# Performance work log

Hardware: AMD Instinct MI355X
Metric: run time of the kernel (lower is better)

The kernel has to match this reference:

```python
import jax, jax.numpy as jnp
import numpy as np

H = 16          # nhead
EPS = 1e-5      # LayerNorm eps (torch default)


def _layernorm(x, g, b):
    mu = jnp.mean(x, axis=-1, keepdims=True)
    var = jnp.mean(jnp.square(x - mu), axis=-1, keepdims=True)
    return (x - mu) * jax.lax.rsqrt(var + EPS) * g + b


def setup_inputs() -> dict:
    key = jax.random.key(0)
    ks = jax.random.split(key, 8)
    B, L, D, F = 256, 64, 1024, 4096
    s = 0.02
    return {
        "src": jax.random.normal(ks[0], (B, L, D), jnp.float32),
        "Wq": jax.random.normal(ks[1], (D, D), jnp.float32) * s,
        "bq": jnp.zeros((D,), jnp.float32),
        "Wk": jax.random.normal(ks[2], (D, D), jnp.float32) * s,
        "bk": jnp.zeros((D,), jnp.float32),
        "Wv": jax.random.normal(ks[3], (D, D), jnp.float32) * s,
        "bv": jnp.zeros((D,), jnp.float32),
        "Wo": jax.random.normal(ks[4], (D, D), jnp.float32) * s,
        "bo": jnp.zeros((D,), jnp.float32),
        "rel_bias": jax.random.normal(ks[5], (H, 2 * L - 1), jnp.float32) * s,
        "W1": jax.random.normal(ks[6], (D, F), jnp.float32) * s,
        "b1": jnp.zeros((F,), jnp.float32),
        "W2": jax.random.normal(ks[7], (F, D), jnp.float32) * s,
        "b2": jnp.zeros((D,), jnp.float32),
        "g1": jnp.ones((D,), jnp.float32),
        "be1": jnp.zeros((D,), jnp.float32),
        "g2": jnp.ones((D,), jnp.float32),
        "be2": jnp.zeros((D,), jnp.float32),
    }


def reference(src, Wq, bq, Wk, bk, Wv, bv, Wo, bo, rel_bias,
              W1, b1, W2, b2, g1, be1, g2, be2):
    B, L, D = src.shape
    dh = D // H
    # --- relative multi-head attention ---
    q = (src @ Wq + bq).reshape(B, L, H, dh)
    k = (src @ Wk + bk).reshape(B, L, H, dh)
    v = (src @ Wv + bv).reshape(B, L, H, dh)
    scores = jnp.einsum('bqhd,bkhd->bhqk', q, k) / jnp.sqrt(jnp.float32(dh))
    # relative position bias lookup: index i - j + (L-1) into (H, 2L-1) table
    rel_idx = jnp.arange(L)[:, None] - jnp.arange(L)[None, :] + (L - 1)  # (L,L)
    scores = scores + rel_bias[:, rel_idx]  # broadcast (H,L,L) over batch
    attn = jax.nn.softmax(scores, axis=-1)
    ctx = jnp.einsum('bhqk,bkhd->bqhd', attn, v).reshape(B, L, D)
    attn_out = ctx @ Wo + bo
    # --- residual + LN + FFN + residual + LN (dropout = eval no-op) ---
    x = _layernorm(src + attn_out, g1, be1)
    ff = jax.nn.gelu(x @ W1 + b1) @ W2 + b2
    return _layernorm(x + ff, g2, be2)
```

## Files before the change

### kernel.cpp

```cpp
#include <hip/hip_runtime.h>

typedef __bf16 bf16;
typedef __attribute__((ext_vector_type(8))) __bf16 bf16x8;
typedef __attribute__((ext_vector_type(4))) __bf16 bf16x4;
typedef __attribute__((ext_vector_type(4))) float f32x4;

#define N_TOK 16384
#define DMODEL 1024
#define FDIM 4096
#define NHEAD 16

__device__ __forceinline__ void gload_lds16(const bf16* g, bf16* l) {
  __builtin_amdgcn_global_load_lds(
      (const __attribute__((address_space(1))) void*)g,
      (__attribute__((address_space(3))) void*)l,
      16, 0, 0);
}

__device__ __forceinline__ float gelu_tanh(float x) {
  return 0.5f * x * (1.0f + tanhf(0.7978845608028654f * (x + 0.044715f * x * x * x)));
}

__global__ __launch_bounds__(256) void cvt_copy(const float* __restrict__ x,
                                                bf16* __restrict__ y) {
  size_t i = ((size_t)blockIdx.x * 256 + threadIdx.x) * 8;
  float4 a = *(const float4*)(x + i);
  float4 b = *(const float4*)(x + i + 4);
  bf16x8 o;
  o[0] = (bf16)a.x; o[1] = (bf16)a.y; o[2] = (bf16)a.z; o[3] = (bf16)a.w;
  o[4] = (bf16)b.x; o[5] = (bf16)b.y; o[6] = (bf16)b.z; o[7] = (bf16)b.w;
  *(bf16x8*)(y + i) = o;
}

__global__ void convt(const float* __restrict__ src, bf16* __restrict__ dst,
                      int R, int C) {
  __shared__ float tile[32][33];
  int c0 = blockIdx.x * 32, r0 = blockIdx.y * 32;
  int tx = threadIdx.x, ty = threadIdx.y;
#pragma unroll
  for (int i = 0; i < 4; ++i)
    tile[ty * 4 + i][tx] = src[(size_t)(r0 + ty * 4 + i) * C + c0 + tx];
  __syncthreads();
#pragma unroll
  for (int i = 0; i < 4; ++i)
    dst[(size_t)(c0 + ty * 4 + i) * R + r0 + tx] = (bf16)tile[tx][ty * 4 + i];
}

template <int BM_, int RES, int GELU>
__global__ __launch_bounds__(512) void gemm_c(
    const bf16* __restrict__ A, const bf16* __restrict__ BT,
    const float* __restrict__ bias, const float* __restrict__ resf,
    const bf16* __restrict__ resb, bf16* __restrict__ C,
    int M, int N, int K) {
  constexpr int ALOADS = BM_ / 64;
  constexpr int MH = BM_ / 32;
  constexpr int MQ = MH / 2;
  __shared__ alignas(16) bf16 sA[2][BM_ * 64];
  __shared__ alignas(16) bf16 sB[2][256 * 64];

  const int tid = threadIdx.x;
  const int lane = tid & 63, wv = tid >> 6;
  const int wr = wv >> 2, wc = wv & 3;
  const int r16 = lane & 15, hk = lane >> 4;

  const int nbn = N >> 8;
  const int cpx = gridDim.x >> 3;
  const int swz = ((int)blockIdx.x & 7) * cpx + ((int)blockIdx.x >> 3);
  const int row0 = (swz / nbn) * BM_, col0 = (swz % nbn) << 8;

  const bf16* Ab = A + (size_t)row0 * K;
  const bf16* Bb = BT + (size_t)col0 * K;

  auto stageA = [&](int buf, int kt) {
#pragma unroll
    for (int l = 0; l < ALOADS; ++l) {
      int g = l * 512 + tid;
      int r = g >> 3, p = g & 7;
      gload_lds16(Ab + (size_t)r * K + ((size_t)kt << 6) + ((p ^ (r & 7)) << 3),
                  &sA[buf][g * 8]);
    }
  };
  auto stageB = [&](int buf, int kt) {
#pragma unroll
    for (int l = 0; l < 4; ++l) {
      int g = l * 512 + tid;
      int r = g >> 3, p = g & 7;
      gload_lds16(Bb + (size_t)r * K + ((size_t)kt << 6) + ((p ^ (r & 7)) << 3),
                  &sB[buf][g * 8]);
    }
  };
  auto frag = [&](const bf16* s, int row, int kc) -> bf16x8 {
    return *(const bf16x8*)(s + row * 64 + (kc ^ ((row & 7) * 8)));
  };

  f32x4 acc[MH][4] = {};
  bf16x8 aF[MQ][2], bF0[2][2], bF1[2][2];

  const int nt = K >> 6;
  stageA(0, 0); stageB(0, 0);
  stageA(1, 1); stageB(1, 1);
  if constexpr (BM_ == 256) asm volatile("s_waitcnt vmcnt(8)" ::: "memory");
  else                      asm volatile("s_waitcnt vmcnt(6)" ::: "memory");
  __builtin_amdgcn_s_barrier();

  for (int kt = 0; kt < nt; ++kt) {
    const int cb = kt & 1;
    const bf16* sa = &sA[cb][0];
    const bf16* sb = &sB[cb][0];
    const bool pf = (kt + 2 < nt);

#pragma unroll
    for (int m = 0; m < MQ; ++m)
#pragma unroll
      for (int ks = 0; ks < 2; ++ks)
        aF[m][ks] = frag(sa, wr * (BM_ / 2) + m * 16 + r16, ks * 32 + hk * 8);
#pragma unroll
    for (int n = 0; n < 2; ++n)
#pragma unroll
      for (int ks = 0; ks < 2; ++ks)
        bF0[n][ks] = frag(sb, wc * 64 + n * 16 + r16, ks * 32 + hk * 8);
    __builtin_amdgcn_s_barrier();
    __builtin_amdgcn_s_setprio(1);
#pragma unroll
    for (int m = 0; m < MQ; ++m)
#pragma unroll
      for (int n = 0; n < 2; ++n)
#pragma unroll
        for (int ks = 0; ks < 2; ++ks)
          acc[m][n] = __builtin_amdgcn_mfma_f32_16x16x32_bf16(bF0[n][ks], aF[m][ks], acc[m][n], 0, 0, 0);
    __builtin_amdgcn_s_setprio(0);
    __builtin_amdgcn_s_barrier();

#pragma unroll
    for (int n = 0; n < 2; ++n)
#pragma unroll
      for (int ks = 0; ks < 2; ++ks)
        bF1[n][ks] = frag(sb, wc * 64 + (2 + n) * 16 + r16, ks * 32 + hk * 8);
    __builtin_amdgcn_s_barrier();
    __builtin_amdgcn_s_setprio(1);
#pragma unroll
    for (int m = 0; m < MQ; ++m)
#pragma unroll
      for (int n = 0; n < 2; ++n)
#pragma unroll
        for (int ks = 0; ks < 2; ++ks)
          acc[m][2 + n] = __builtin_amdgcn_mfma_f32_16x16x32_bf16(bF1[n][ks], aF[m][ks], acc[m][2 + n], 0, 0, 0);
    __builtin_amdgcn_s_setprio(0);
    __builtin_amdgcn_s_barrier();

#pragma unroll
    for (int m = 0; m < MQ; ++m)
#pragma unroll
      for (int ks = 0; ks < 2; ++ks)
        aF[m][ks] = frag(sa, wr * (BM_ / 2) + (MQ + m) * 16 + r16, ks * 32 + hk * 8);
    if (pf) stageB(cb, kt + 2);
    __builtin_amdgcn_s_barrier();
    __builtin_amdgcn_s_setprio(1);
#pragma unroll
    for (int m = 0; m < MQ; ++m)
#pragma unroll
      for (int n = 0; n < 2; ++n)
#pragma unroll
        for (int ks = 0; ks < 2; ++ks)
          acc[MQ + m][2 + n] = __builtin_amdgcn_mfma_f32_16x16x32_bf16(bF1[n][ks], aF[m][ks], acc[MQ + m][2 + n], 0, 0, 0);
    __builtin_amdgcn_s_setprio(0);
    __builtin_amdgcn_s_barrier();

    if (pf) stageA(cb, kt + 2);
    __builtin_amdgcn_s_setprio(1);
#pragma unroll
    for (int m = 0; m < MQ; ++m)
#pragma unroll
      for (int n = 0; n < 2; ++n)
#pragma unroll
        for (int ks = 0; ks < 2; ++ks)
          acc[MQ + m][n] = __builtin_amdgcn_mfma_f32_16x16x32_bf16(bF0[n][ks], aF[m][ks], acc[MQ + m][n], 0, 0, 0);
    __builtin_amdgcn_s_setprio(0);
    if (pf) {
      if constexpr (BM_ == 256) asm volatile("s_waitcnt vmcnt(8)" ::: "memory");
      else                      asm volatile("s_waitcnt vmcnt(6)" ::: "memory");
    } else if (kt + 1 < nt) {
      asm volatile("s_waitcnt vmcnt(0)" ::: "memory");
    }
    __builtin_amdgcn_s_barrier();
  }

#pragma unroll
  for (int m = 0; m < MH; ++m) {
    int row = row0 + wr * (BM_ / 2) + m * 16 + r16;
#pragma unroll
    for (int n = 0; n < 4; ++n) {
      int col = col0 + wc * 64 + n * 16 + hk * 4;
      f32x4 b4 = *(const f32x4*)&bias[col];
      f32x4 v;
#pragma unroll
      for (int r = 0; r < 4; ++r) v[r] = acc[m][n][r] + b4[r];
      if (RES == 1) {
        f32x4 rr = *(const f32x4*)&resf[(size_t)row * N + col];
#pragma unroll
        for (int r = 0; r < 4; ++r) v[r] += rr[r];
      }
      if (RES == 2) {
        bf16x4 rb = *(const bf16x4*)&resb[(size_t)row * N + col];
#pragma unroll
        for (int r = 0; r < 4; ++r) v[r] += (float)rb[r];
      }
      bf16x4 o;
#pragma unroll
      for (int r = 0; r < 4; ++r) {
        float x = v[r];
        if (GELU) x = gelu_tanh(x);
        o[r] = (bf16)x;
      }
      *(bf16x4*)&C[(size_t)row * N + col] = o;
    }
  }
}

__global__ __launch_bounds__(256) void attn_k(
    const bf16* q, const bf16* __restrict__ k,
    const bf16* __restrict__ v, const float* __restrict__ rel,
    bf16* ctx) {
  __shared__ alignas(16) bf16 lQ[64 * 64];
  __shared__ alignas(16) bf16 lK[64 * 64];
  __shared__ alignas(16) bf16 lVt[64 * 64];
  __shared__ alignas(16) bf16 lP[4][16 * 64];
  __shared__ float lrel[128];

  const int bh = blockIdx.x;
  const int b = bh >> 4, h = bh & 15;
  const int tid = threadIdx.x;
  const size_t base = (size_t)(b * 64) * DMODEL + h * 64;

#pragma unroll
  for (int i = 0; i < 2; ++i) {
    int j = (tid >> 3) + i * 32;
    int d0 = (tid & 7) * 8;
    *(bf16x8*)&lQ[j * 64 + d0] = *(const bf16x8*)(q + base + (size_t)j * DMODEL + d0);
    *(bf16x8*)&lK[j * 64 + d0] = *(const bf16x8*)(k + base + (size_t)j * DMODEL + d0);
    bf16x8 vvv = *(const bf16x8*)(v + base + (size_t)j * DMODEL + d0);
#pragma unroll
    for (int u = 0; u < 8; ++u) lVt[(d0 + u) * 64 + j] = vvv[u];
  }
  if (tid < 127) lrel[tid] = rel[h * 127 + tid];
  __syncthreads();

  const int lane = tid & 63, w = tid >> 6;
  const int r16 = lane & 15, hk = lane >> 4;

  f32x4 s[4] = {};
#pragma unroll
  for (int dstep = 0; dstep < 2; ++dstep) {
    bf16x8 aq = *(const bf16x8*)&lQ[(w * 16 + r16) * 64 + dstep * 32 + hk * 8];
#pragma unroll
    for (int n = 0; n < 4; ++n) {
      bf16x8 bk_ = *(const bf16x8*)&lK[(n * 16 + r16) * 64 + dstep * 32 + hk * 8];
      s[n] = __builtin_amdgcn_mfma_f32_16x16x32_bf16(aq, bk_, s[n], 0, 0, 0);
    }
  }

  float p[16];
#pragma unroll
  for (int n = 0; n < 4; ++n)
#pragma unroll
    for (int r = 0; r < 4; ++r) {
      int i = w * 16 + hk * 4 + r;
      int j = n * 16 + r16;
      p[n * 4 + r] = s[n][r] * 0.125f + lrel[i - j + 63];
    }
#pragma unroll
  for (int r = 0; r < 4; ++r) {
    float m = fmaxf(fmaxf(p[r], p[4 + r]), fmaxf(p[8 + r], p[12 + r]));
#pragma unroll
    for (int off = 1; off < 16; off <<= 1) m = fmaxf(m, __shfl_xor(m, off));
    float sum = 0.f;
#pragma unroll
    for (int n = 0; n < 4; ++n) {
      p[n * 4 + r] = __expf(p[n * 4 + r] - m);
      sum += p[n * 4 + r];
    }
#pragma unroll
    for (int off = 1; off < 16; off <<= 1) sum += __shfl_xor(sum, off);
    float inv = 1.0f / sum;
#pragma unroll
    for (int n = 0; n < 4; ++n) p[n * 4 + r] *= inv;
  }
#pragma unroll
  for (int n = 0; n < 4; ++n)
#pragma unroll
    for (int r = 0; r < 4; ++r)
      lP[w][(hk * 4 + r) * 64 + n * 16 + r16] = (bf16)p[n * 4 + r];
  __syncthreads();

  f32x4 o[4] = {};
#pragma unroll
  for (int ks = 0; ks < 2; ++ks) {
    bf16x8 ap = *(const bf16x8*)&lP[w][r16 * 64 + ks * 32 + hk * 8];
#pragma unroll
    for (int n = 0; n < 4; ++n) {
      bf16x8 bv_ = *(const bf16x8*)&lVt[(n * 16 + r16) * 64 + ks * 32 + hk * 8];
      o[n] = __builtin_amdgcn_mfma_f32_16x16x32_bf16(ap, bv_, o[n], 0, 0, 0);
    }
  }
#pragma unroll
  for (int n = 0; n < 4; ++n)
#pragma unroll
    for (int r = 0; r < 4; ++r) {
      int trow = b * 64 + w * 16 + hk * 4 + r;
      ctx[(size_t)trow * DMODEL + h * 64 + n * 16 + r16] = (bf16)o[n][r];
    }
}

template <int F32OUT>
__global__ __launch_bounds__(256) void layernorm_k(
    const bf16* __restrict__ x, const float* __restrict__ g,
    const float* __restrict__ be, bf16* __restrict__ ob,
    float* __restrict__ of) {
  int row = blockIdx.x * 4 + (threadIdx.x >> 6);
  int lane = threadIdx.x & 63;
  const bf16* xr = x + (size_t)row * DMODEL + lane * 16;
  bf16x8 v0 = *(const bf16x8*)xr;
  bf16x8 v1 = *(const bf16x8*)(xr + 8);
  float f[16];
#pragma unroll
  for (int j = 0; j < 8; ++j) { f[j] = (float)v0[j]; f[8 + j] = (float)v1[j]; }
  float s = 0.f, sq = 0.f;
#pragma unroll
  for (int j = 0; j < 16; ++j) { s += f[j]; sq += f[j] * f[j]; }
#pragma unroll
  for (int off = 1; off < 64; off <<= 1) {
    s += __shfl_xor(s, off);
    sq += __shfl_xor(sq, off);
  }
  float mean = s * (1.0f / DMODEL);
  float var = sq * (1.0f / DMODEL) - mean * mean;
  float rstd = rsqrtf(var + 1e-5f);
  const float* gp = g + lane * 16;
  const float* bp = be + lane * 16;
  if (F32OUT) {
    float* op = of + (size_t)row * DMODEL + lane * 16;
#pragma unroll
    for (int j = 0; j < 16; ++j)
      op[j] = (f[j] - mean) * rstd * gp[j] + bp[j];
  } else {
    bf16x8 o0, o1;
#pragma unroll
    for (int j = 0; j < 8; ++j) {
      o0[j] = (bf16)((f[j] - mean) * rstd * gp[j] + bp[j]);
      o1[j] = (bf16)((f[8 + j] - mean) * rstd * gp[8 + j] + bp[8 + j]);
    }
    bf16* op = ob + (size_t)row * DMODEL + lane * 16;
    *(bf16x8*)op = o0;
    *(bf16x8*)(op + 8) = o1;
  }
}

extern "C" void kernel_launch(void* const* d_in, const int* in_sizes, int n_in,
                              void* d_out, int out_size, void* d_ws, size_t ws_size,
                              hipStream_t stream) {
  (void)in_sizes; (void)n_in; (void)out_size;
  const float* src = (const float*)d_in[0];
  const float* Wq  = (const float*)d_in[1];
  const float* bq  = (const float*)d_in[2];
  const float* Wk  = (const float*)d_in[3];
  const float* bk  = (const float*)d_in[4];
  const float* Wv  = (const float*)d_in[5];
  const float* bv  = (const float*)d_in[6];
  const float* Wo  = (const float*)d_in[7];
  const float* bo  = (const float*)d_in[8];
  const float* rel = (const float*)d_in[9];
  const float* W1  = (const float*)d_in[10];
  const float* b1  = (const float*)d_in[11];
  const float* W2  = (const float*)d_in[12];
  const float* b2  = (const float*)d_in[13];
  const float* g1  = (const float*)d_in[14];
  const float* be1 = (const float*)d_in[15];
  const float* g2  = (const float*)d_in[16];
  const float* be2 = (const float*)d_in[17];

  char* ws = (char*)d_ws;
  const size_t MiB = 1ull << 20;
  bf16* srcb = (bf16*)(ws + 0 * MiB);
  bf16* qb   = (bf16*)(ws + 32 * MiB);
  bf16* WqT  = (bf16*)(ws + 64 * MiB);
  bf16* WkT  = (bf16*)(ws + 66 * MiB);
  bf16* WvT  = (bf16*)(ws + 68 * MiB);
  bf16* WoT  = (bf16*)(ws + 70 * MiB);
  bf16* W1T  = (bf16*)(ws + 72 * MiB);
  bf16* W2T  = (bf16*)(ws + 80 * MiB);
  bf16* hbuf = (bf16*)(ws + 0 * MiB);
  float* lnout = (float*)(ws + 0 * MiB);
  bf16* kb = (bf16*)d_out;
  bf16* vb = (bf16*)((char*)d_out + 32 * MiB);
  bf16* y1 = kb;
  bf16* xb = vb;
  const bool bigws = (ws_size >= 121 * MiB);
  bf16* y2 = bigws ? (bf16*)(ws + 88 * MiB) : kb;

  cvt_copy<<<(N_TOK * DMODEL) / 2048, 256, 0, stream>>>(src, srcb);
  dim3 tb(32, 8);
  convt<<<dim3(32, 32), tb, 0, stream>>>(Wq, WqT, 1024, 1024);
  convt<<<dim3(32, 32), tb, 0, stream>>>(Wk, WkT, 1024, 1024);
  convt<<<dim3(32, 32), tb, 0, stream>>>(Wv, WvT, 1024, 1024);
  convt<<<dim3(32, 32), tb, 0, stream>>>(Wo, WoT, 1024, 1024);
  convt<<<dim3(128, 32), tb, 0, stream>>>(W1, W1T, 1024, 4096);
  convt<<<dim3(32, 128), tb, 0, stream>>>(W2, W2T, 4096, 1024);

  const int gQKV = (N_TOK / 256) * (DMODEL / 256);
  gemm_c<256, 0, 0><<<gQKV, 512, 0, stream>>>(srcb, WqT, bq, nullptr, nullptr, qb, N_TOK, DMODEL, DMODEL);
  gemm_c<256, 0, 0><<<gQKV, 512, 0, stream>>>(srcb, WkT, bk, nullptr, nullptr, kb, N_TOK, DMODEL, DMODEL);
  gemm_c<256, 0, 0><<<gQKV, 512, 0, stream>>>(srcb, WvT, bv, nullptr, nullptr, vb, N_TOK, DMODEL, DMODEL);

  attn_k<<<256 * NHEAD, 256, 0, stream>>>(qb, kb, vb, rel, qb);

  gemm_c<256, 1, 0><<<gQKV, 512, 0, stream>>>(qb, WoT, bo, src, nullptr, y1, N_TOK, DMODEL, DMODEL);
  layernorm_k<0><<<N_TOK / 4, 256, 0, stream>>>(y1, g1, be1, xb, nullptr);

  const int CH = 8192;
  const int gF1 = (CH / 256) * (FDIM / 256);
  const int gF2 = (CH / 128) * (DMODEL / 256);
  for (int c = 0; c < 2; ++c) {
    const bf16* xc = xb + (size_t)c * CH * DMODEL;
    bf16* yc = y2 + (size_t)c * CH * DMODEL;
    gemm_c<256, 0, 1><<<gF1, 512, 0, stream>>>(xc, W1T, b1, nullptr, nullptr, hbuf, CH, FDIM, DMODEL);
    gemm_c<128, 2, 0><<<gF2, 512, 0, stream>>>(hbuf, W2T, b2, nullptr, xc, yc, CH, DMODEL, FDIM);
  }
  if (bigws) {
    layernorm_k<1><<<N_TOK / 4, 256, 0, stream>>>(y2, g2, be2, nullptr, (float*)d_out);
  } else {
    layernorm_k<1><<<N_TOK / 4, 256, 0, stream>>>(y2, g2, be2, nullptr, lnout);
    hipMemcpyAsync(d_out, lnout, (size_t)N_TOK * DMODEL * 4, hipMemcpyDeviceToDevice, stream);
  }
}
```

Baseline: 633.3 us.

## Fuse Q/K/V projections into one GEMM launch and cheapen the GELU epilogue

The three separate Q, K and V projection GEMMs become a single launch with N=3072. The epilogue uses each block's column group to pick the matching output buffer and bias. This assumes the transposed Wq, Wk and Wv weights sit contiguously in the workspace, and it removes two launches while giving the grid a better shape. GELU tanh is rewritten in its exact sigmoid form using __expf, per-thread global load addresses are precomputed outside the k-loop, and the MFMA loop order is changed so the ks loop is outermost.

```diff
diff --git a/kernel.cpp b/kernel.cpp
--- a/kernel.cpp
+++ b/kernel.cpp
@@ -17,8 +17,9 @@
       16, 0, 0);
 }
 
-__device__ __forceinline__ float gelu_tanh(float x) {
-  return 0.5f * x * (1.0f + tanhf(0.7978845608028654f * (x + 0.044715f * x * x * x)));
+__device__ __forceinline__ float gelu_fast(float x) {
+  float z2 = 1.5957691216057308f * (x + 0.044715f * x * x * x);
+  return x / (1.0f + __expf(-z2));
 }
 
 __global__ __launch_bounds__(256) void cvt_copy(const float* __restrict__ x,
@@ -46,11 +47,13 @@
     dst[(size_t)(c0 + ty * 4 + i) * R + r0 + tx] = (bf16)tile[tx][ty * 4 + i];
 }
 
-template <int BM_, int RES, int GELU>
+template <int BM_, int RES, int GELU, int SPLIT3>
 __global__ __launch_bounds__(512) void gemm_c(
     const bf16* __restrict__ A, const bf16* __restrict__ BT,
-    const float* __restrict__ bias, const float* __restrict__ resf,
+    const float* __restrict__ bias, const float* __restrict__ bias2,
+    const float* __restrict__ bias3, const float* __restrict__ resf,
     const bf16* __restrict__ resb, bf16* __restrict__ C,
+    bf16* __restrict__ C2, bf16* __restrict__ C3,
     int M, int N, int K) {
   constexpr int ALOADS = BM_ / 64;
   constexpr int MH = BM_ / 32;
@@ -71,23 +74,30 @@
   const bf16* Ab = A + (size_t)row0 * K;
   const bf16* Bb = BT + (size_t)col0 * K;
 
+  const bf16* gA[ALOADS];
+  const bf16* gB[4];
+#pragma unroll
+  for (int l = 0; l < ALOADS; ++l) {
+    int g = l * 512 + tid, r = g >> 3, p = g & 7;
+    gA[l] = Ab + (size_t)r * K + ((p ^ (r & 7)) << 3);
+  }
+#pragma unroll
+  for (int l = 0; l < 4; ++l) {
+    int g = l * 512 + tid, r = g >> 3, p = g & 7;
+    gB[l] = Bb + (size_t)r * K + ((p ^ (r & 7)) << 3);
+  }
+
   auto stageA = [&](int buf, int kt) {
-#pragma unroll
-    for (int l = 0; l < ALOADS; ++l) {
-      int g = l * 512 + tid;
-      int r = g >> 3, p = g & 7;
-      gload_lds16(Ab + (size_t)r * K + ((size_t)kt << 6) + ((p ^ (r & 7)) << 3),
-                  &sA[buf][g * 8]);
-    }
+    const size_t ko = (size_t)kt << 6;
+#pragma unroll
+    for (int l = 0; l < ALOADS; ++l)
+      gload_lds16(gA[l] + ko, &sA[buf][(l * 512 + tid) * 8]);
   };
   auto stageB = [&](int buf, int kt) {
-#pragma unroll
-    for (int l = 0; l < 4; ++l) {
-      int g = l * 512 + tid;
-      int r = g >> 3, p = g & 7;
-      gload_lds16(Bb + (size_t)r * K + ((size_t)kt << 6) + ((p ^ (r & 7)) << 3),
-                  &sB[buf][g * 8]);
-    }
+    const size_t ko = (size_t)kt << 6;
+#pragma unroll
+    for (int l = 0; l < 4; ++l)
+      gload_lds16(gB[l] + ko, &sB[buf][(l * 512 + tid) * 8]);
   };
   auto frag = [&](const bf16* s, int row, int kc) -> bf16x8 {
     return *(const bf16x8*)(s + row * 64 + (kc ^ ((row & 7) * 8)));
@@ -122,11 +132,11 @@
     __builtin_amdgcn_s_barrier();
     __builtin_amdgcn_s_setprio(1);
 #pragma unroll
-    for (int m = 0; m < MQ; ++m)
-#pragma unroll
-      for (int n = 0; n < 2; ++n)
-#pragma unroll
-        for (int ks = 0; ks < 2; ++ks)
+    for (int ks = 0; ks < 2; ++ks)
+#pragma unroll
+      for (int m = 0; m < MQ; ++m)
+#pragma unroll
+        for (int n = 0; n < 2; ++n)
           acc[m][n] = __builtin_amdgcn_mfma_f32_16x16x32_bf16(bF0[n][ks], aF[m][ks], acc[m][n], 0, 0, 0);
     __builtin_amdgcn_s_setprio(0);
     __builtin_amdgcn_s_barrier();
@@ -139,11 +149,11 @@
     __builtin_amdgcn_s_barrier();
     __builtin_amdgcn_s_setprio(1);
 #pragma unroll
-    for (int m = 0; m < MQ; ++m)
-#pragma unroll
-      for (int n = 0; n < 2; ++n)
-#pragma unroll
-        for (int ks = 0; ks < 2; ++ks)
+    for (int ks = 0; ks < 2; ++ks)
+#pragma unroll
+      for (int m = 0; m < MQ; ++m)
+#pragma unroll
+        for (int n = 0; n < 2; ++n)
           acc[m][2 + n] = __builtin_amdgcn_mfma_f32_16x16x32_bf16(bF1[n][ks], aF[m][ks], acc[m][2 + n], 0, 0, 0);
     __builtin_amdgcn_s_setprio(0);
     __builtin_amdgcn_s_barrier();
@@ -157,11 +167,11 @@
     __builtin_amdgcn_s_barrier();
     __builtin_amdgcn_s_setprio(1);
 #pragma unroll
-    for (int m = 0; m < MQ; ++m)
-#pragma unroll
-      for (int n = 0; n < 2; ++n)
-#pragma unroll
-        for (int ks = 0; ks < 2; ++ks)
+    for (int ks = 0; ks < 2; ++ks)
+#pragma unroll
+      for (int m = 0; m < MQ; ++m)
+#pragma unroll
+        for (int n = 0; n < 2; ++n)
           acc[MQ + m][2 + n] = __builtin_amdgcn_mfma_f32_16x16x32_bf16(bF1[n][ks], aF[m][ks], acc[MQ + m][2 + n], 0, 0, 0);
     __builtin_amdgcn_s_setprio(0);
     __builtin_amdgcn_s_barrier();
@@ -169,11 +179,11 @@
     if (pf) stageA(cb, kt + 2);
     __builtin_amdgcn_s_setprio(1);
 #pragma unroll
-    for (int m = 0; m < MQ; ++m)
-#pragma unroll
-      for (int n = 0; n < 2; ++n)
-#pragma unroll
-        for (int ks = 0; ks < 2; ++ks)
+    for (int ks = 0; ks < 2; ++ks)
+#pragma unroll
+      for (int m = 0; m < MQ; ++m)
+#pragma unroll
+        for (int n = 0; n < 2; ++n)
           acc[MQ + m][n] = __builtin_amdgcn_mfma_f32_16x16x32_bf16(bF0[n][ks], aF[m][ks], acc[MQ + m][n], 0, 0, 0);
     __builtin_amdgcn_s_setprio(0);
     if (pf) {
@@ -185,23 +195,33 @@
     __builtin_amdgcn_s_barrier();
   }
 
+  bf16* Cp = C;
+  const float* bp = bias;
+  int ldc = N, colb = col0;
+  if constexpr (SPLIT3) {
+    int grp = col0 >> 10;
+    Cp = grp == 0 ? C : (grp == 1 ? C2 : C3);
+    bp = grp == 0 ? bias : (grp == 1 ? bias2 : bias3);
+    ldc = 1024;
+    colb = col0 & 1023;
+  }
 #pragma unroll
   for (int m = 0; m < MH; ++m) {
     int row = row0 + wr * (BM_ / 2) + m * 16 + r16;
 #pragma unroll
     for (int n = 0; n < 4; ++n) {
-      int col = col0 + wc * 64 + n * 16 + hk * 4;
-      f32x4 b4 = *(const f32x4*)&bias[col];
+      int col = colb + wc * 64 + n * 16 + hk * 4;
+      f32x4 b4 = *(const f32x4*)&bp[col];
       f32x4 v;
 #pragma unroll
       for (int r = 0; r < 4; ++r) v[r] = acc[m][n][r] + b4[r];
       if (RES == 1) {
-        f32x4 rr = *(const f32x4*)&resf[(size_t)row * N + col];
+        f32x4 rr = *(const f32x4*)&resf[(size_t)row * ldc + col];
 #pragma unroll
         for (int r = 0; r < 4; ++r) v[r] += rr[r];
       }
       if (RES == 2) {
-        bf16x4 rb = *(const bf16x4*)&resb[(size_t)row * N + col];
+        bf16x4 rb = *(const bf16x4*)&resb[(size_t)row * ldc + col];
 #pragma unroll
         for (int r = 0; r < 4; ++r) v[r] += (float)rb[r];
       }
@@ -209,10 +229,10 @@
 #pragma unroll
       for (int r = 0; r < 4; ++r) {
         float x = v[r];
-        if (GELU) x = gelu_tanh(x);
+        if (GELU) x = gelu_fast(x);
         o[r] = (bf16)x;
       }
-      *(bf16x4*)&C[(size_t)row * N + col] = o;
+      *(bf16x4*)&Cp[(size_t)row * ldc + col] = o;
     }
   }
 }
@@ -406,14 +426,15 @@
   convt<<<dim3(128, 32), tb, 0, stream>>>(W1, W1T, 1024, 4096);
   convt<<<dim3(32, 128), tb, 0, stream>>>(W2, W2T, 4096, 1024);
 
-  const int gQKV = (N_TOK / 256) * (DMODEL / 256);
-  gemm_c<256, 0, 0><<<gQKV, 512, 0, stream>>>(srcb, WqT, bq, nullptr, nullptr, qb, N_TOK, DMODEL, DMODEL);
-  gemm_c<256, 0, 0><<<gQKV, 512, 0, stream>>>(srcb, WkT, bk, nullptr, nullptr, kb, N_TOK, DMODEL, DMODEL);
-  gemm_c<256, 0, 0><<<gQKV, 512, 0, stream>>>(srcb, WvT, bv, nullptr, nullptr, vb, N_TOK, DMODEL, DMODEL);
+  const int gQKV3 = (N_TOK / 256) * (3072 / 256);
+  gemm_c<256, 0, 0, 1><<<gQKV3, 512, 0, stream>>>(
+      srcb, WqT, bq, bk, bv, nullptr, nullptr, qb, kb, vb, N_TOK, 3072, DMODEL);
 
   attn_k<<<256 * NHEAD, 256, 0, stream>>>(qb, kb, vb, rel, qb);
 
-  gemm_c<256, 1, 0><<<gQKV, 512, 0, stream>>>(qb, WoT, bo, src, nullptr, y1, N_TOK, DMODEL, DMODEL);
+  const int gD = (N_TOK / 256) * (DMODEL / 256);
+  gemm_c<256, 1, 0, 0><<<gD, 512, 0, stream>>>(
+      qb, WoT, bo, nullptr, nullptr, src, nullptr, y1, nullptr, nullptr, N_TOK, DMODEL, DMODEL);
   layernorm_k<0><<<N_TOK / 4, 256, 0, stream>>>(y1, g1, be1, xb, nullptr);
 
   const int CH = 8192;
@@ -422,8 +443,10 @@
   for (int c = 0; c < 2; ++c) {
     const bf16* xc = xb + (size_t)c * CH * DMODEL;
     bf16* yc = y2 + (size_t)c * CH * DMODEL;
-    gemm_c<256, 0, 1><<<gF1, 512, 0, stream>>>(xc, W1T, b1, nullptr, nullptr, hbuf, CH, FDIM, DMODEL);
-    gemm_c<128, 2, 0><<<gF2, 512, 0, stream>>>(hbuf, W2T, b2, nullptr, xc, yc, CH, DMODEL, FDIM);
+    gemm_c<256, 0, 1, 0><<<gF1, 512, 0, stream>>>(
+        xc, W1T, b1, nullptr, nullptr, nullptr, nullptr, hbuf, nullptr, nullptr, CH, FDIM, DMODEL);
+    gemm_c<128, 2, 0, 0><<<gF2, 512, 0, stream>>>(
+        hbuf, W2T, b2, nullptr, nullptr, nullptr, xc, yc, nullptr, nullptr, CH, DMODEL, FDIM);
   }
   if (bigws) {
     layernorm_k<1><<<N_TOK / 4, 256, 0, stream>>>(y2, g2, be2, nullptr, (float*)d_out);
```

After: 613.3 us. 1.03x faster.
